# Kernel tuning notes

Hardware: AMD Instinct MI355X
Metric: run time of the kernel (lower is better)

The kernel has to match this reference:

```python
import jax, jax.numpy as jnp
import numpy as np

N_HEADS = 32
N_KV_HEADS = 8
HEAD_DIM = 128
HIDDEN = 4096
EPS = 1e-5
ROPE_BASE = 10000.0


def _per_head_layernorm(x, w, eps=EPS):
    # x: [B, S, nH, D], w: [nH, D]; LayerNorm over head_dim, weight only (no bias)
    mean = jnp.mean(x, axis=-1, keepdims=True)
    var = jnp.mean(jnp.square(x - mean), axis=-1, keepdims=True)
    return (x - mean) * jax.lax.rsqrt(var + eps) * w[None, None, :, :]


def _apply_rope(x, cos, sin):
    # x: [B, S, nH, D]; cos/sin: [1, S, 1, D/2]; GPT-NeoX half-split rotation
    d2 = x.shape[-1] // 2
    x1, x2 = x[..., :d2], x[..., d2:]
    return jnp.concatenate([x1 * cos - x2 * sin, x2 * cos + x1 * sin], axis=-1)


def setup_inputs() -> dict:
    key = jax.random.key(0)
    ks = jax.random.split(key, 6)
    B, S = 2, 2048
    return {
        "hidden_states": jax.random.normal(ks[0], (B, S, HIDDEN), jnp.float32),
        "position_ids": jnp.arange(S, dtype=jnp.int32),
        "wq": jax.random.normal(ks[1], (N_HEADS * HEAD_DIM, HIDDEN), jnp.float32) * 0.02,
        "wk": jax.random.normal(ks[2], (N_KV_HEADS * HEAD_DIM, HIDDEN), jnp.float32) * 0.02,
        "wv": jax.random.normal(ks[3], (N_KV_HEADS * HEAD_DIM, HIDDEN), jnp.float32) * 0.02,
        "wo": jax.random.normal(ks[4], (HIDDEN, N_HEADS * HEAD_DIM), jnp.float32) * 0.02,
        "q_norm_w": jnp.ones((N_HEADS, HEAD_DIM), jnp.float32),
        "k_norm_w": jnp.ones((N_KV_HEADS, HEAD_DIM), jnp.float32),
    }


def reference(hidden_states, position_ids, wq, wk, wv, wo, q_norm_w, k_norm_w):
    B, S, H = hidden_states.shape
    # fused QKV projection (column-packed q_proj|k_proj|v_proj)
    q = (hidden_states @ wq.T).reshape(B, S, N_HEADS, HEAD_DIM)
    k = (hidden_states @ wk.T).reshape(B, S, N_KV_HEADS, HEAD_DIM)
    v = (hidden_states @ wv.T).reshape(B, S, N_KV_HEADS, HEAD_DIM)
    # per-head QK LayerNorm (Cohere-style)
    q = _per_head_layernorm(q, q_norm_w)
    k = _per_head_layernorm(k, k_norm_w)
    # rotary embedding, base 10000, dim = head_dim
    inv_freq = 1.0 / (ROPE_BASE ** (jnp.arange(0, HEAD_DIM, 2, dtype=jnp.float32) / HEAD_DIM))
    ang = position_ids.astype(jnp.float32)[:, None] * inv_freq  # [S, D/2]
    cos = jnp.cos(ang)[None, :, None, :]
    sin = jnp.sin(ang)[None, :, None, :]
    q = _apply_rope(q, cos, sin)
    k = _apply_rope(k, cos, sin)
    # GQA expansion via kv_head_mapping = arange(n_kv).repeat_interleave(groups)
    groups = N_HEADS // N_KV_HEADS
    k = jnp.repeat(k, groups, axis=2)  # [B, S, nH, D]
    v = jnp.repeat(v, groups, axis=2)
    # causal attention
    scale = HEAD_DIM ** -0.5
    scores = jnp.einsum("bqhd,bkhd->bhqk", q, k) * scale
    causal = jnp.tril(jnp.ones((S, S), dtype=bool))
    scores = jnp.where(causal[None, None], scores, jnp.finfo(scores.dtype).min)
    probs = jax.nn.softmax(scores, axis=-1)
    attn = jnp.einsum("bhqk,bkhd->bqhd", probs, v).reshape(B, S, N_HEADS * HEAD_DIM)
    return attn @ wo.T
```

## Files before the change

kernel.cpp:

```cpp
#include <hip/hip_runtime.h>
#include <hip/hip_bf16.h>
#include <stdint.h>
#include <math.h>

typedef __bf16 bf16;
typedef __bf16 bf16x4 __attribute__((ext_vector_type(4)));
typedef __bf16 bf16x8 __attribute__((ext_vector_type(8)));
typedef float  f32x4  __attribute__((ext_vector_type(4)));
typedef float  f32x16 __attribute__((ext_vector_type(16)));

#define HIDDEN 4096
#define NH     32
#define NKV    8
#define HD     128
#define SEQ    2048
#define BATCH  2
#define NTOK   (BATCH*SEQ)
#define QDIM   (NH*HD)
#define KVDIM  (NKV*HD)

#define NEGBIG (-3.0e38f)

__device__ __forceinline__ void gl_lds16(const bf16* g, bf16* l) {
    __builtin_amdgcn_global_load_lds((__attribute__((address_space(1))) void*)g,
                                     (__attribute__((address_space(3))) void*)l,
                                     16, 0, 0);
}

__global__ __launch_bounds__(256)
void cvt_f32_bf16(const float* __restrict__ src, bf16* __restrict__ dst)
{
    const size_t i = ((size_t)blockIdx.x * 256 + threadIdx.x) * 8;
    f32x4 f0 = *(const f32x4*)(src + i);
    f32x4 f1 = *(const f32x4*)(src + i + 4);
    bf16x8 o;
    #pragma unroll
    for (int j = 0; j < 4; ++j) { o[j] = (bf16)f0[j]; o[4+j] = (bf16)f1[j]; }
    *(bf16x8*)(dst + i) = o;
}

template<int MODE>
__global__ __launch_bounds__(256)
void gemm_bt(const bf16* __restrict__ A, const bf16* __restrict__ B,
             void* __restrict__ Cv, void* __restrict__ Cv2, int M, int N, int K)
{
    __shared__ bf16 sA[128*32];
    __shared__ bf16 sB[128*32];

    const int tid  = threadIdx.x;
    const int wave = tid >> 6;
    const int lane = tid & 63;
    const int l15  = lane & 15;
    const int quad = lane >> 4;
    const int m_blk = blockIdx.y * 128;
    const int n_blk = blockIdx.x * 128;
    const int wm = (wave >> 1) * 64;
    const int wn = (wave & 1) * 64;

    f32x4 acc[4][4] = {};

    const int rowInSeg = lane >> 2;
    const int colInSeg = (lane & 3) * 8;

    for (int k0 = 0; k0 < K; k0 += 32) {
        __syncthreads();
        #pragma unroll
        for (int i = 0; i < 2; ++i) {
            int s = wave * 2 + i;
            const bf16* ga = A + (size_t)(m_blk + s*16 + rowInSeg) * K + k0 + colInSeg;
            gl_lds16(ga, sA + s*512);
            const bf16* gb = B + (size_t)(n_blk + s*16 + rowInSeg) * K + k0 + colInSeg;
            gl_lds16(gb, sB + s*512);
        }
        __syncthreads();

        bf16x8 af[4], bfr[4];
        #pragma unroll
        for (int mi = 0; mi < 4; ++mi)
            af[mi] = *(const bf16x8*)(sA + (wm + mi*16 + l15)*32 + quad*8);
        #pragma unroll
        for (int ni = 0; ni < 4; ++ni)
            bfr[ni] = *(const bf16x8*)(sB + (wn + ni*16 + l15)*32 + quad*8);
        #pragma unroll
        for (int mi = 0; mi < 4; ++mi)
            #pragma unroll
            for (int ni = 0; ni < 4; ++ni)
                acc[mi][ni] = __builtin_amdgcn_mfma_f32_16x16x32_bf16(
                                  af[mi], bfr[ni], acc[mi][ni], 0, 0, 0);
    }

    #pragma unroll
    for (int mi = 0; mi < 4; ++mi) {
        #pragma unroll
        for (int ni = 0; ni < 4; ++ni) {
            const int col = n_blk + wn + ni*16 + l15;
            const int row0 = m_blk + wm + mi*16 + quad*4;
            if constexpr (MODE == 2) {
                const int bb = row0 >> 11;
                const int ss = row0 & (SEQ - 1);
                bf16x4 pk;
                #pragma unroll
                for (int r = 0; r < 4; ++r) pk[r] = (bf16)acc[mi][ni][r];
                *(bf16x4*)((bf16*)Cv + ((size_t)bb * KVDIM + col) * SEQ + ss) = pk;
            } else if constexpr (MODE == 1) {
                #pragma unroll
                for (int r = 0; r < 4; ++r)
                    ((float*)Cv)[(size_t)(row0 + r) * N + col] = acc[mi][ni][r];
            } else if constexpr (MODE == 3) {
                if (n_blk < KVDIM) {
                    #pragma unroll
                    for (int r = 0; r < 4; ++r)
                        ((bf16*)Cv)[(size_t)(row0 + r) * KVDIM + col] = (bf16)acc[mi][ni][r];
                } else {
                    const int vcol = col - KVDIM;
                    const int bb = row0 >> 11;
                    const int ss = row0 & (SEQ - 1);
                    bf16x4 pk;
                    #pragma unroll
                    for (int r = 0; r < 4; ++r) pk[r] = (bf16)acc[mi][ni][r];
                    *(bf16x4*)((bf16*)Cv2 + ((size_t)bb * KVDIM + vcol) * SEQ + ss) = pk;
                }
            } else {
                #pragma unroll
                for (int r = 0; r < 4; ++r)
                    ((bf16*)Cv)[(size_t)(row0 + r) * N + col] = (bf16)acc[mi][ni][r];
            }
        }
    }
}

#define LDB(p, qn, bf) { const char* base_ = (const char*)sB[p]; \
    _Pragma("unroll") for (int ni = 0; ni < 2; ++ni) \
    _Pragma("unroll") for (int ks = 0; ks < 2; ++ks) \
        bf[ni][ks] = *(const bf16x8*)(base_ + (wn + (qn)*32 + ni*16 + l15)*128 \
                                      + ((ks*64 + quad*16) ^ kx)); }

#define LDA(p, qm) { const char* base_ = (const char*)sA[p]; \
    _Pragma("unroll") for (int mi = 0; mi < 4; ++mi) \
    _Pragma("unroll") for (int ks = 0; ks < 2; ++ks) \
        af[mi][ks] = *(const bf16x8*)(base_ + (wm + (qm)*64 + mi*16 + l15)*128 \
                                      + ((ks*64 + quad*16) ^ kx)); }

#define MM(qm, qn, bf) { \
    _Pragma("unroll") for (int mi = 0; mi < 4; ++mi) \
    _Pragma("unroll") for (int ni = 0; ni < 2; ++ni) \
    _Pragma("unroll") for (int ks = 0; ks < 2; ++ks) \
        acc[(qm)*4+mi][(qn)*2+ni] = __builtin_amdgcn_mfma_f32_16x16x32_bf16( \
            af[mi][ks], bf[ni][ks], acc[(qm)*4+mi][(qn)*2+ni], 0, 0, 0); }

#define MIDBAR() { __builtin_amdgcn_s_barrier(); \
    asm volatile("s_waitcnt lgkmcnt(0)" ::: "memory"); \
    __builtin_amdgcn_sched_barrier(0); \
    __builtin_amdgcn_s_setprio(1); }

#define ENDBAR() { __builtin_amdgcn_s_setprio(0); \
    __builtin_amdgcn_sched_barrier(0); \
    __builtin_amdgcn_s_barrier(); }

#define ENDBAR_VM(n) { __builtin_amdgcn_s_setprio(0); \
    __builtin_amdgcn_sched_barrier(0); \
    asm volatile("s_waitcnt vmcnt(" #n ")" ::: "memory"); \
    __builtin_amdgcn_s_barrier(); }

template<bool F32OUT>
__global__ __launch_bounds__(512)
void gemm256(const bf16* __restrict__ A, const bf16* __restrict__ B,
             void* __restrict__ Cv, int M, int N, int K)
{
    __shared__ bf16 sA[2][256*64];
    __shared__ bf16 sB[2][256*64];

    const int tid  = threadIdx.x;
    const int wave = tid >> 6;
    const int lane = tid & 63;
    const int l15  = lane & 15;
    const int quad = lane >> 4;
    const int m_blk = blockIdx.y * 256;
    const int n_blk = blockIdx.x * 256;
    const int wm = (wave >> 2) * 128;
    const int wn = (wave & 3) * 64;
    const int kx = (l15 & 7) << 4;

    const bf16* Ag = A + (size_t)m_blk * K;
    const bf16* Bg = B + (size_t)n_blk * K;

    const int rs  = lane >> 3;
    const int sg8 = ((lane & 7) ^ rs) * 8;

    f32x4 acc[8][4] = {};

    auto stA = [&](int p, int h, int k0) {
        bf16* sb = sA[p];
        const int r0 = h*64 + wave*8;
        const int r1 = r0 + 128;
        gl_lds16(Ag + (size_t)(r0 + rs)*K + k0 + sg8, sb + r0*64);
        gl_lds16(Ag + (size_t)(r1 + rs)*K + k0 + sg8, sb + r1*64);
    };
    auto stB = [&](int p, int h, int k0) {
        bf16* sb = sB[p];
        #pragma unroll
        for (int j = 0; j < 2; ++j) {
            const int s  = j*8 + wave;
            const int rb = (s>>2)*64 + h*32 + (s&3)*8;
            gl_lds16(Bg + (size_t)(rb + rs)*K + k0 + sg8, sb + rb*64);
        }
    };

    bf16x8 af[4][2], b0[2][2], b1[2][2];

    stA(0, 0, 0);  stA(0, 1, 0);  stB(0, 0, 0);  stB(0, 1, 0);
    stA(1, 0, 64); stB(1, 0, 64); stB(1, 1, 64);
    asm volatile("s_waitcnt vmcnt(6)" ::: "memory");
    __builtin_amdgcn_s_barrier();

    const int niter = K >> 7;
    for (int it = 0; it < niter; ++it) {
        const int kc  = it << 7;
        const bool pre = (it + 1 < niter);

        LDA(0, 0); LDB(0, 0, b0);
        stA(1, 1, kc + 64);
        MIDBAR(); MM(0, 0, b0); ENDBAR();

        LDB(0, 1, b1);
        if (pre) stA(0, 0, kc + 128);
        MIDBAR(); MM(0, 1, b1); ENDBAR();

        LDA(0, 1);
        if (pre) stB(0, 0, kc + 128);
        MIDBAR(); MM(1, 0, b0); ENDBAR();

        if (pre) stB(0, 1, kc + 128);
        MIDBAR(); MM(1, 1, b1);
        if (pre) { ENDBAR_VM(6); } else { ENDBAR_VM(0); }

        LDA(1, 0); LDB(1, 0, b0);
        if (pre) stA(0, 1, kc + 128);
        MIDBAR(); MM(0, 0, b0); ENDBAR();

        LDB(1, 1, b1);
        if (pre) stA(1, 0, kc + 192);
        MIDBAR(); MM(0, 1, b1); ENDBAR();

        LDA(1, 1);
        if (pre) stB(1, 0, kc + 192);
        MIDBAR(); MM(1, 0, b0); ENDBAR();

        if (pre) stB(1, 1, kc + 192);
        MIDBAR(); MM(1, 1, b1);
        if (pre) { ENDBAR_VM(6); } else { ENDBAR(); }
    }

    #pragma unroll
    for (int ai = 0; ai < 8; ++ai) {
        const int row0 = m_blk + wm + (ai>>2)*64 + (ai&3)*16 + quad*4;
        #pragma unroll
        for (int bi = 0; bi < 4; ++bi) {
            const int col = n_blk + wn + (bi>>1)*32 + (bi&1)*16 + l15;
            if constexpr (F32OUT) {
                #pragma unroll
                for (int r = 0; r < 4; ++r)
                    ((float*)Cv)[(size_t)(row0 + r)*N + col] = acc[ai][bi][r];
            } else {
                #pragma unroll
                for (int r = 0; r < 4; ++r)
                    ((bf16*)Cv)[(size_t)(row0 + r)*N + col] = (bf16)acc[ai][bi][r];
            }
        }
    }
}

__global__ __launch_bounds__(256)
void ln_rope(bf16* __restrict__ buf, const float* __restrict__ w,
             const int* __restrict__ pos, int nh)
{
    const int id   = blockIdx.x * 4 + (threadIdx.x >> 6);
    const int lane = threadIdx.x & 63;
    const int t  = id / nh;
    const int hh = id - t * nh;

    bf16* p = buf + (size_t)t * nh * HD + hh * HD;
    float x1 = (float)p[lane];
    float x2 = (float)p[lane + 64];

    float s1 = x1 + x2, s2 = x1*x1 + x2*x2;
    #pragma unroll
    for (int m = 1; m < 64; m <<= 1) {
        s1 += __shfl_xor(s1, m);
        s2 += __shfl_xor(s2, m);
    }
    const float mean = s1 * (1.0f/128.0f);
    const float var  = s2 * (1.0f/128.0f) - mean*mean;
    const float rs   = rsqrtf(fmaxf(var, 0.0f) + 1e-5f);

    const float w1 = w[hh*HD + lane];
    const float w2 = w[hh*HD + lane + 64];
    const float xn1 = (x1 - mean) * rs * w1;
    const float xn2 = (x2 - mean) * rs * w2;

    const int s = t & (SEQ - 1);
    const float ang = (float)pos[s] * __expf(-(float)lane * (9.210340371976184f/64.0f));
    const float c = cosf(ang), sn = sinf(ang);

    p[lane]      = (bf16)(xn1 * c - xn2 * sn);
    p[lane + 64] = (bf16)(xn2 * c + xn1 * sn);
}

struct StReg { bf16x8 k0, k1, v0, v1; };

__device__ __forceinline__ StReg stage_load(const bf16* kgp, const bf16* vgp, int t)
{
    StReg r;
    const size_t ko = (size_t)t * 64 * KVDIM;
    r.k0 = *(const bf16x8*)(kgp + ko);
    r.k1 = *(const bf16x8*)(kgp + ko + 64);
    r.v0 = *(const bf16x8*)(vgp + t*64);
    r.v1 = *(const bf16x8*)(vgp + t*64 + 32);
    return r;
}

__device__ __forceinline__ void stage_write(bf16* dk, bf16* dv, const StReg& r,
                                            int krow, int kcb, int vrow, int vcb)
{
    *(bf16x8*)((char*)dk + krow*256 + ( kcb        ^ ((krow&7)<<4))) = r.k0;
    *(bf16x8*)((char*)dk + krow*256 + ((kcb + 128) ^ ((krow&7)<<4))) = r.k1;
    *(bf16x8*)((char*)dv + vrow*128 + ( vcb        ^ ((vrow&7)<<4))) = r.v0;
    *(bf16x8*)((char*)dv + vrow*128 + ((vcb +  64) ^ ((vrow&7)<<4))) = r.v1;
}

__device__ __forceinline__ unsigned pk2(float x, float y)
{
    union { bf16 h[2]; unsigned u; } c;
    c.h[0] = (bf16)x; c.h[1] = (bf16)y;
    return c.u;
}

__global__ __launch_bounds__(512, 2)
void attn_fa(bf16* __restrict__ qob,
             const bf16* __restrict__ kbp,
             const bf16* __restrict__ vtb)
{
    __shared__ bf16 sK[2][64*128];
    __shared__ bf16 sV[2][128*64];

    const int tid  = threadIdx.x;
    const int wave = tid >> 6;
    const int lane = tid & 63;
    const int l31  = lane & 31;
    const int hi   = lane >> 5;

    const int b  = blockIdx.z;
    const int qt = b ? (gridDim.x - 1 - blockIdx.x) : blockIdx.x;
    const int h  = blockIdx.y;
    const int hk = h >> 2;
    const int qbase = qt * 256;
    const int qw    = qbase + wave * 32;
    const int qrow  = qw + l31;

    bf16x8 qf[8];
    {
        const bf16* qp = qob + (size_t)(b*SEQ + qrow)*QDIM + h*HD + hi*8;
        #pragma unroll
        for (int ks = 0; ks < 8; ++ks)
            qf[ks] = *(const bf16x8*)(qp + ks*16);
    }

    f32x16 oacc[4] = {};
    float m_i = NEGBIG, l_i = 0.0f;

    const int krow = tid >> 3;
    const int kcb  = (tid & 7) * 16;
    const int vrow = tid >> 2;
    const int vcb  = (tid & 3) * 16;
    const bf16* kgp = kbp + (size_t)(b*SEQ + krow)*KVDIM + hk*HD + (tid & 7)*8;
    const bf16* vgp = vtb + ((size_t)(b*NKV + hk)*HD + vrow)*SEQ + (tid & 3)*8;

    const int ntiles = qt*4 + 4;
    const float SC = 0.08838834764831845f * 1.4426950408889634f;
    const int kx = (l31 & 7) << 4;

    {
        StReg r = stage_load(kgp, vgp, 0);
        stage_write(sK[0], sV[0], r, krow, kcb, vrow, vcb);
    }
    __syncthreads();

    int cur = 0;
    for (int t = 0; t < ntiles; ++t) {
        const int kv0 = t * 64;
        const bool hn = (t + 1 < ntiles);
        StReg nx;
        if (hn) nx = stage_load(kgp, vgp, t + 1);

        if (kv0 <= qw + 31) {
            f32x16 sa0 = {}, sa1 = {};
            const char* kl = (const char*)sK[cur];
            __builtin_amdgcn_s_setprio(1);
            #pragma unroll
            for (int ks = 0; ks < 8; ++ks) {
                const int cb = ks*32 + hi*16;
                bf16x8 k0 = *(const bf16x8*)(kl + l31*256        + (cb ^ kx));
                bf16x8 k1 = *(const bf16x8*)(kl + l31*256 + 8192 + (cb ^ kx));
                sa0 = __builtin_amdgcn_mfma_f32_32x32x16_bf16(k0, qf[ks], sa0, 0, 0, 0);
                sa1 = __builtin_amdgcn_mfma_f32_32x32x16_bf16(k1, qf[ks], sa1, 0, 0, 0);
            }
            __builtin_amdgcn_s_setprio(0);

            float s[32];
            #pragma unroll
            for (int r = 0; r < 16; ++r) { s[r] = sa0[r]*SC; s[16+r] = sa1[r]*SC; }
            if (kv0 + 63 > qw) {
                #pragma unroll
                for (int j = 0; j < 32; ++j) {
                    const int kv = kv0 + (j>>4)*32 + (j&3) + ((j>>2)&3)*8 + hi*4;
                    if (kv > qrow) s[j] = NEGBIG;
                }
            }

            float mt = s[0];
            #pragma unroll
            for (int j = 1; j < 32; ++j) mt = fmaxf(mt, s[j]);
            mt = fmaxf(mt, __shfl_xor(mt, 32));
            if (__any(mt > m_i + 8.0f)) {
                const float mnew = fmaxf(m_i, mt);
                const float al = exp2f(m_i - mnew);
                m_i = mnew; l_i *= al;
                #pragma unroll
                for (int d = 0; d < 4; ++d)
                    #pragma unroll
                    for (int r = 0; r < 16; ++r) oacc[d][r] *= al;
            }
            float p[32]; float sum = 0.0f;
            #pragma unroll
            for (int j = 0; j < 32; ++j) { p[j] = exp2f(s[j] - m_i); sum += p[j]; }
            sum += __shfl_xor(sum, 32);
            l_i += sum;

            bf16x8 pb[4];
            #pragma unroll
            for (int ks = 0; ks < 4; ++ks) {
                const int c = (ks>>1)*16 + (ks&1)*8;
                const unsigned a0 = pk2(p[c+0], p[c+1]);
                const unsigned a1 = pk2(p[c+2], p[c+3]);
                const unsigned b0 = pk2(p[c+4], p[c+5]);
                const unsigned b1 = pk2(p[c+6], p[c+7]);
                const unsigned r0 = (unsigned)__shfl_xor((int)(hi ? a0 : b0), 32);
                const unsigned r1 = (unsigned)__shfl_xor((int)(hi ? a1 : b1), 32);
                union { unsigned u[4]; bf16x8 v; } fr;
                fr.u[0] = hi ? r0 : a0;
                fr.u[1] = hi ? r1 : a1;
                fr.u[2] = hi ? b0 : r0;
                fr.u[3] = hi ? b1 : r1;
                pb[ks] = fr.v;
            }

            const char* vl = (const char*)sV[cur];
            __builtin_amdgcn_s_setprio(1);
            #pragma unroll
            for (int d = 0; d < 4; ++d) {
                #pragma unroll
                for (int ks = 0; ks < 4; ++ks) {
                    const int cb = ks*32 + hi*16;
                    bf16x8 vf = *(const bf16x8*)(vl + (d*32 + l31)*128 + (cb ^ kx));
                    oacc[d] = __builtin_amdgcn_mfma_f32_32x32x16_bf16(vf, pb[ks], oacc[d], 0, 0, 0);
                }
            }
            __builtin_amdgcn_s_setprio(0);
        }

        if (hn) stage_write(sK[cur^1], sV[cur^1], nx, krow, kcb, vrow, vcb);
        __syncthreads();
        cur ^= 1;
    }

    const float inv = 1.0f / l_i;
    bf16* op = qob + (size_t)(b*SEQ + qrow)*QDIM + h*HD + hi*4;
    #pragma unroll
    for (int d = 0; d < 4; ++d) {
        #pragma unroll
        for (int q2 = 0; q2 < 4; ++q2) {
            bf16x4 pk;
            #pragma unroll
            for (int r = 0; r < 4; ++r) pk[r] = (bf16)(oacc[d][q2*4 + r] * inv);
            *(bf16x4*)(op + d*32 + q2*8) = pk;
        }
    }
}

extern "C" void kernel_launch(void* const* d_in, const int* in_sizes, int n_in,
                              void* d_out, int out_size, void* d_ws, size_t ws_size,
                              hipStream_t stream)
{
    const float* hidden = (const float*)d_in[0];
    const int*   pos    = (const int*)d_in[1];
    const float* wq     = (const float*)d_in[2];
    const float* wk     = (const float*)d_in[3];
    const float* wv     = (const float*)d_in[4];
    const float* wo     = (const float*)d_in[5];
    const float* qw     = (const float*)d_in[6];
    const float* kw     = (const float*)d_in[7];

    bf16* hb   = (bf16*)d_ws;
    bf16* wqb  = hb   + (size_t)NTOK*HIDDEN;
    bf16* wkb  = wqb  + (size_t)QDIM*HIDDEN;
    bf16* wvb  = wkb  + (size_t)KVDIM*HIDDEN;
    bf16* qbuf = wvb  + (size_t)KVDIM*HIDDEN;
    bf16* kbuf = qbuf + (size_t)NTOK*QDIM;
    bf16* vtb  = kbuf + (size_t)NTOK*KVDIM;
    float* out = (float*)d_out;

    const dim3 blk(256);

    cvt_f32_bf16<<<dim3(NTOK*HIDDEN/2048),  blk, 0, stream>>>(hidden, hb);
    cvt_f32_bf16<<<dim3(QDIM*HIDDEN/2048),  blk, 0, stream>>>(wq, wqb);
    cvt_f32_bf16<<<dim3(KVDIM*HIDDEN/2048), blk, 0, stream>>>(wk, wkb);
    cvt_f32_bf16<<<dim3(KVDIM*HIDDEN/2048), blk, 0, stream>>>(wv, wvb);

    gemm256<false><<<dim3(QDIM/256, NTOK/256), dim3(512), 0, stream>>>(hb, wqb, qbuf, NTOK, QDIM, HIDDEN);

    gemm_bt<3><<<dim3((2*KVDIM)/128, NTOK/128), blk, 0, stream>>>(hb, wkb, kbuf, vtb, NTOK, 2*KVDIM, HIDDEN);

    cvt_f32_bf16<<<dim3(QDIM*HIDDEN/2048), blk, 0, stream>>>(wo, wqb);

    ln_rope<<<dim3(NTOK*NH/4),  blk, 0, stream>>>(qbuf, qw, pos, NH);
    ln_rope<<<dim3(NTOK*NKV/4), blk, 0, stream>>>(kbuf, kw, pos, NKV);

    attn_fa<<<dim3(SEQ/256, NH, BATCH), dim3(512), 0, stream>>>(qbuf, kbuf, vtb);

    gemm256<true><<<dim3(QDIM/256, NTOK/256), dim3(512), 0, stream>>>(qbuf, wqb, out, NTOK, QDIM, HIDDEN);
}
```

Baseline: 721.4 us.

## Software-pipeline LDS fragment loads in gemm256 to overlap with MFMA phases

Restructures the gemm256 main loop so that the LDS-to-register fragment loads for the next MFMA phase are issued inside the current phase, with MFMA work running while the reads are in flight. Double A-fragment registers (afA/afB) let one set be read while the other is used. The global-load wait points move earlier (vmcnt 4) so the next buffer's data is ready before its fragments are prefetched. This raises register pressure and relies on the MIDBAR lgkmcnt wait placement, so the added loads may serialize anyway or cut occupancy.

```diff
diff --git a/kernel.cpp b/kernel.cpp
--- a/kernel.cpp
+++ b/kernel.cpp
@@ -129,24 +129,24 @@
     }
 }
 
-#define LDB(p, qn, bf) { const char* base_ = (const char*)sB[p]; \
+#define LDB2(p, qn, dst) { const char* base_ = (const char*)sB[p]; \
     _Pragma("unroll") for (int ni = 0; ni < 2; ++ni) \
     _Pragma("unroll") for (int ks = 0; ks < 2; ++ks) \
-        bf[ni][ks] = *(const bf16x8*)(base_ + (wn + (qn)*32 + ni*16 + l15)*128 \
+        dst[ni][ks] = *(const bf16x8*)(base_ + (wn + (qn)*32 + ni*16 + l15)*128 \
                                       + ((ks*64 + quad*16) ^ kx)); }
 
-#define LDA(p, qm) { const char* base_ = (const char*)sA[p]; \
+#define LDA2(p, qm, dst) { const char* base_ = (const char*)sA[p]; \
     _Pragma("unroll") for (int mi = 0; mi < 4; ++mi) \
     _Pragma("unroll") for (int ks = 0; ks < 2; ++ks) \
-        af[mi][ks] = *(const bf16x8*)(base_ + (wm + (qm)*64 + mi*16 + l15)*128 \
+        dst[mi][ks] = *(const bf16x8*)(base_ + (wm + (qm)*64 + mi*16 + l15)*128 \
                                       + ((ks*64 + quad*16) ^ kx)); }
 
-#define MM(qm, qn, bf) { \
+#define MM2(qm, qn, a, bf) { \
     _Pragma("unroll") for (int mi = 0; mi < 4; ++mi) \
     _Pragma("unroll") for (int ni = 0; ni < 2; ++ni) \
     _Pragma("unroll") for (int ks = 0; ks < 2; ++ks) \
         acc[(qm)*4+mi][(qn)*2+ni] = __builtin_amdgcn_mfma_f32_16x16x32_bf16( \
-            af[mi][ks], bf[ni][ks], acc[(qm)*4+mi][(qn)*2+ni], 0, 0, 0); }
+            a[mi][ks], bf[ni][ks], acc[(qm)*4+mi][(qn)*2+ni], 0, 0, 0); }
 
 #define MIDBAR() { __builtin_amdgcn_s_barrier(); \
     asm volatile("s_waitcnt lgkmcnt(0)" ::: "memory"); \
@@ -206,49 +206,58 @@
         }
     };
 
-    bf16x8 af[4][2], b0[2][2], b1[2][2];
+    bf16x8 afA[4][2], afB[4][2], b0[2][2], b1[2][2];
 
     stA(0, 0, 0);  stA(0, 1, 0);  stB(0, 0, 0);  stB(0, 1, 0);
     stA(1, 0, 64); stB(1, 0, 64); stB(1, 1, 64);
     asm volatile("s_waitcnt vmcnt(6)" ::: "memory");
     __builtin_amdgcn_s_barrier();
+    LDA2(0, 0, afA); LDB2(0, 0, b0);
 
     const int niter = K >> 7;
     for (int it = 0; it < niter; ++it) {
         const int kc  = it << 7;
         const bool pre = (it + 1 < niter);
 
-        LDA(0, 0); LDB(0, 0, b0);
         stA(1, 1, kc + 64);
-        MIDBAR(); MM(0, 0, b0); ENDBAR();
-
-        LDB(0, 1, b1);
+        MIDBAR();
+        LDB2(0, 1, b1);
+        MM2(0, 0, afA, b0); ENDBAR();
+
         if (pre) stA(0, 0, kc + 128);
-        MIDBAR(); MM(0, 1, b1); ENDBAR();
-
-        LDA(0, 1);
+        MIDBAR();
+        LDA2(0, 1, afB);
+        MM2(0, 1, afA, b1); ENDBAR();
+
         if (pre) stB(0, 0, kc + 128);
-        MIDBAR(); MM(1, 0, b0); ENDBAR();
+        MIDBAR();
+        MM2(1, 0, afB, b0);
+        if (pre) { ENDBAR_VM(4); } else { ENDBAR_VM(0); }
 
         if (pre) stB(0, 1, kc + 128);
-        MIDBAR(); MM(1, 1, b1);
-        if (pre) { ENDBAR_VM(6); } else { ENDBAR_VM(0); }
-
-        LDA(1, 0); LDB(1, 0, b0);
+        MIDBAR();
+        LDA2(1, 0, afA); LDB2(1, 0, b0);
+        MM2(1, 1, afB, b1); ENDBAR();
+
         if (pre) stA(0, 1, kc + 128);
-        MIDBAR(); MM(0, 0, b0); ENDBAR();
-
-        LDB(1, 1, b1);
+        MIDBAR();
+        LDB2(1, 1, b1);
+        MM2(0, 0, afA, b0); ENDBAR();
+
         if (pre) stA(1, 0, kc + 192);
-        MIDBAR(); MM(0, 1, b1); ENDBAR();
-
-        LDA(1, 1);
+        MIDBAR();
+        LDA2(1, 1, afB);
+        MM2(0, 1, afA, b1); ENDBAR();
+
         if (pre) stB(1, 0, kc + 192);
-        MIDBAR(); MM(1, 0, b0); ENDBAR();
+        MIDBAR();
+        MM2(1, 0, afB, b0);
+        if (pre) { ENDBAR_VM(4); } else { ENDBAR(); }
 
         if (pre) stB(1, 1, kc + 192);
-        MIDBAR(); MM(1, 1, b1);
-        if (pre) { ENDBAR_VM(6); } else { ENDBAR(); }
+        MIDBAR();
+        if (pre) { LDA2(0, 0, afA); LDB2(0, 0, b0); }
+        MM2(1, 1, afB, b1); ENDBAR();
     }
 
     #pragma unroll
```

Result: slower. 886.4 us (+22.9%).
